# Kernel tuning notes

Hardware: AMD Instinct MI355X
Metric: run time of the kernel (lower is better)

The kernel has to match this reference:

```python
import jax, jax.numpy as jnp
import numpy as np

N = 50000
E = 800000
D_IN = 128
HID = 128
LAT = 64
NEG_SLOPE = 0.2


def setup_inputs() -> dict:
    key = jax.random.key(0)
    ks = jax.random.split(key, 16)
    g = lambda k, shape: jax.random.normal(k, shape, dtype=jnp.float32) * (1.0 / np.sqrt(shape[0]))
    x = jax.random.normal(ks[0], (N, D_IN), dtype=jnp.float32)
    edge_index = jax.random.randint(ks[1], (2, E), 0, N, dtype=jnp.int64)
    return {
        "x": x,
        "edge_index": edge_index,
        # lin1: Linear(D_IN, HID)
        "lin1_w": g(ks[2], (D_IN, HID)),
        "lin1_b": jnp.zeros((HID,), jnp.float32),
        # conv1: GATConv((D_IN, D_IN) -> HID), heads=1
        "w1_src": g(ks[3], (D_IN, HID)),
        "w1_dst": g(ks[4], (D_IN, HID)),
        "a1_src": g(ks[5], (HID,)),
        "a1_dst": g(ks[6], (HID,)),
        "b1": jnp.zeros((HID,), jnp.float32),
        # conv2: GATConv((HID, HID) -> LAT), heads=1
        "w2_src": g(ks[7], (HID, LAT)),
        "w2_dst": g(ks[8], (HID, LAT)),
        "a2_src": g(ks[9], (LAT,)),
        "a2_dst": g(ks[10], (LAT,)),
        "b2": jnp.zeros((LAT,), jnp.float32),
    }


def _gat_conv(x, src, dst, w_src, w_dst, a_src, a_dst, b):
    """PyG GATConv, heads=1, add_self_loops=False. x: [N, Din]."""
    n = x.shape[0]
    hs = x @ w_src                    # [N, C] messages (source transform)
    hd = x @ w_dst                    # [N, C] destination transform
    alpha_s = hs @ a_src              # [N]
    alpha_d = hd @ a_dst              # [N]
    e = jax.nn.leaky_relu(alpha_s[src] + alpha_d[dst], NEG_SLOPE)  # [E]
    # segment softmax over incoming edges per destination node
    m = jax.ops.segment_max(e, dst, num_segments=n)
    ex = jnp.exp(e - m[dst])
    denom = jax.ops.segment_sum(ex, dst, num_segments=n)
    alpha = ex / (denom[dst] + 1e-16)                              # [E]
    msg = hs[src] * alpha[:, None]                                 # [E, C]
    out = jax.ops.segment_sum(msg, dst, num_segments=n)            # [N, C]
    return out + b


def reference(x, edge_index, lin1_w, lin1_b, w1_src, w1_dst, a1_src, a1_dst, b1,
              w2_src, w2_dst, a2_src, a2_dst, b2):
    src, dst = edge_index[0], edge_index[1]
    z = _gat_conv(x, src, dst, w1_src, w1_dst, a1_src, a1_dst, b1)
    z = jax.nn.relu(z + x @ lin1_w + lin1_b)
    z = _gat_conv(z, src, dst, w2_src, w2_dst, a2_src, a2_dst, b2)
    return z
```

## Files before the change

### kernel.cpp

```cpp
#include <hip/hip_runtime.h>

static constexpr int N_NODES = 50000;
static constexpr int N_EDGES = 800000;
static constexpr int NPART = 8;
static constexpr int PART_SZ = N_NODES / NPART;

typedef __attribute__((ext_vector_type(8))) short bf16x8;
typedef __attribute__((ext_vector_type(4))) float f32x4;

__device__ __forceinline__ float bf2f(unsigned short u) {
  union { unsigned int i; float f; } v; v.i = ((unsigned int)u) << 16; return v.f;
}
__device__ __forceinline__ unsigned short f2bf(float f) {
  union { unsigned int i; float f; } v; v.f = f;
  unsigned int r = (v.i + 0x7fffu + ((v.i >> 16) & 1u)) >> 16;
  return (unsigned short)r;
}
__device__ __forceinline__ int clampN(int v) {
  unsigned u = (unsigned)v; return (u < (unsigned)N_NODES) ? (int)u : 0;
}

__global__ void k_detect(const int* __restrict__ ei, int* __restrict__ flag) {
  if (threadIdx.x == 0 && blockIdx.x == 0) {
    int z = ei[1] | ei[3] | ei[5] | ei[7];
    *flag = (z == 0) ? 1 : 0;
  }
}

__global__ void k_zero_out(float* __restrict__ out, int n) {
  int i = blockIdx.x * 256 + threadIdx.x;
  if (i < n) out[i] = 0.f;
}

__global__ void k_prepw(const float* __restrict__ w1_src, const float* __restrict__ wlin,
                        const float* __restrict__ w2_src,
                        const float* __restrict__ w1_dst, const float* __restrict__ a1_dst,
                        const float* __restrict__ w2_dst, const float* __restrict__ a2_dst,
                        unsigned short* __restrict__ w1T, unsigned short* __restrict__ w2T,
                        float* __restrict__ c1dst, float* __restrict__ c2dst) {
  int idx = blockIdx.x * 256 + threadIdx.x;
  if (idx < 256 * 128) {
    int c = idx >> 7, k = idx & 127;
    float v = (c < 128) ? w1_src[k * 128 + c] : wlin[k * 128 + (c - 128)];
    w1T[idx] = f2bf(v);
  } else if (idx < 256 * 128 + 64 * 128) {
    int r = idx - 256 * 128;
    int c = r >> 7, k = r & 127;
    w2T[r] = f2bf(w2_src[k * 64 + c]);
  } else if (blockIdx.x == 160) {
    int k = threadIdx.x;
    if (k < 128) {
      float s1 = 0.f;
      for (int c = 0; c < 128; ++c) s1 += w1_dst[k * 128 + c] * a1_dst[c];
      c1dst[k] = s1;
      float s2 = 0.f;
      for (int c = 0; c < 64; ++c) s2 += w2_dst[k * 64 + c] * a2_dst[c];
      c2dst[k] = s2;
    }
  }
}

__global__ __launch_bounds__(256) void k_gemm1(
    const float* __restrict__ x, const unsigned short* __restrict__ w1T,
    const float* __restrict__ lin_b,
    unsigned short* __restrict__ hs1, unsigned short* __restrict__ linzb) {
  __shared__ unsigned char aLds[16 * 256];
  int nb = blockIdx.x * 16;
  int tid = threadIdx.x;
#pragma unroll
  for (int i = 0; i < 2; ++i) {
    int t = tid + i * 256;
    int row = t >> 5, q = t & 31;
    float4 v = *(const float4*)(x + (size_t)(nb + row) * 128 + q * 4);
    unsigned int lo = (unsigned)f2bf(v.x) | ((unsigned)f2bf(v.y) << 16);
    unsigned int hi = (unsigned)f2bf(v.z) | ((unsigned)f2bf(v.w) << 16);
    int kb = (q * 8) ^ ((row & 7) << 4);
    *(uint2*)(aLds + row * 256 + kb) = make_uint2(lo, hi);
  }
  __syncthreads();
  int wv = tid >> 6, l = tid & 63;
  int lrow = l & 15, lk = l >> 4;
  bf16x8 bfrag[4][4];
#pragma unroll
  for (int ct = 0; ct < 4; ++ct) {
    int col = wv * 64 + ct * 16 + lrow;
#pragma unroll
    for (int ks = 0; ks < 4; ++ks)
      bfrag[ct][ks] = *(const bf16x8*)(w1T + (size_t)col * 128 + ks * 32 + lk * 8);
  }
  f32x4 acc[4] = {{0.f,0.f,0.f,0.f},{0.f,0.f,0.f,0.f},{0.f,0.f,0.f,0.f},{0.f,0.f,0.f,0.f}};
#pragma unroll
  for (int ks = 0; ks < 4; ++ks) {
    int kb = (ks * 64 + lk * 16) ^ ((lrow & 7) << 4);
    bf16x8 afrag = *(const bf16x8*)(aLds + lrow * 256 + kb);
#pragma unroll
    for (int ct = 0; ct < 4; ++ct)
      acc[ct] = __builtin_amdgcn_mfma_f32_16x16x32_bf16(afrag, bfrag[ct][ks], acc[ct], 0, 0, 0);
  }
#pragma unroll
  for (int ct = 0; ct < 4; ++ct) {
    int col = wv * 64 + ct * 16 + lrow;
#pragma unroll
    for (int j = 0; j < 4; ++j) {
      int row = nb + lk * 4 + j;
      float v = acc[ct][j];
      if (col < 128) hs1[(size_t)row * 128 + col] = f2bf(v);
      else linzb[(size_t)row * 128 + (col - 128)] = f2bf(v + lin_b[col - 128]);
    }
  }
}

__global__ __launch_bounds__(256) void k_gemm2(
    const unsigned short* __restrict__ zb, const unsigned short* __restrict__ w2T,
    unsigned short* __restrict__ hs2) {
  __shared__ unsigned char aLds[64 * 256];
  int nb = blockIdx.x * 64;
  int tid = threadIdx.x;
#pragma unroll
  for (int i = 0; i < 4; ++i) {
    int t = tid + i * 256;
    int row = t >> 4, q = t & 15;
    int grow = nb + row; if (grow >= N_NODES) grow = N_NODES - 1;
    uint4 v = *(const uint4*)(zb + (size_t)grow * 128 + q * 8);
    int kb = (q * 16) ^ ((row & 7) << 4);
    *(uint4*)(aLds + row * 256 + kb) = v;
  }
  __syncthreads();
  int wv = tid >> 6, l = tid & 63;
  int lrow = l & 15, lk = l >> 4;
  bf16x8 bfrag[4][4];
#pragma unroll
  for (int ct = 0; ct < 4; ++ct) {
    int col = ct * 16 + lrow;
#pragma unroll
    for (int ks = 0; ks < 4; ++ks)
      bfrag[ct][ks] = *(const bf16x8*)(w2T + (size_t)col * 128 + ks * 32 + lk * 8);
  }
  f32x4 acc[4] = {{0.f,0.f,0.f,0.f},{0.f,0.f,0.f,0.f},{0.f,0.f,0.f,0.f},{0.f,0.f,0.f,0.f}};
  int arow = wv * 16 + lrow;
#pragma unroll
  for (int ks = 0; ks < 4; ++ks) {
    int kb = (ks * 64 + lk * 16) ^ ((arow & 7) << 4);
    bf16x8 afrag = *(const bf16x8*)(aLds + arow * 256 + kb);
#pragma unroll
    for (int ct = 0; ct < 4; ++ct)
      acc[ct] = __builtin_amdgcn_mfma_f32_16x16x32_bf16(afrag, bfrag[ct][ks], acc[ct], 0, 0, 0);
  }
#pragma unroll
  for (int ct = 0; ct < 4; ++ct) {
    int col = ct * 16 + lrow;
#pragma unroll
    for (int j = 0; j < 4; ++j) {
      int row = nb + wv * 16 + lk * 4 + j;
      if (row < N_NODES) hs2[(size_t)row * 64 + col] = f2bf(acc[ct][j]);
    }
  }
}

template <int C, bool XBF>
__global__ __launch_bounds__(256) void k_alpha(
    const unsigned short* __restrict__ hs, const float* __restrict__ asrc,
    const void* __restrict__ xin, const float* __restrict__ cdst,
    float* __restrict__ as_, float* __restrict__ ad_) {
  int node = (int)((blockIdx.x * 256 + threadIdx.x) >> 6);
  if (node >= N_NODES) return;
  int lane = threadIdx.x & 63;
  float sa = 0.f;
#pragma unroll
  for (int k = lane; k < C; k += 64) sa += bf2f(hs[(size_t)node * C + k]) * asrc[k];
  float sd = 0.f;
  if (XBF) {
    const unsigned short* xb = (const unsigned short*)xin;
#pragma unroll
    for (int k = lane; k < 128; k += 64) sd += bf2f(xb[(size_t)node * 128 + k]) * cdst[k];
  } else {
    const float* xf = (const float*)xin;
#pragma unroll
    for (int k = lane; k < 128; k += 64) sd += xf[(size_t)node * 128 + k] * cdst[k];
  }
#pragma unroll
  for (int o = 32; o > 0; o >>= 1) {
    sa += __shfl_xor(sa, o, 64);
    sd += __shfl_xor(sd, o, 64);
  }
  if (lane == 0) { as_[node] = sa; ad_[node] = sd; }
}

__global__ void k_count(const int* __restrict__ ei, const int* __restrict__ flag,
                        int* __restrict__ deg) {
  int part = blockIdx.x & (NPART - 1);
  int e = (blockIdx.x >> 3) * 256 + threadIdx.x;
  if (e < N_EDGES) {
    int f = *flag;
    int d = clampN(ei[(size_t)(N_EDGES + e) << f]);
    int lo = part * PART_SZ;
    if (d >= lo && d < lo + PART_SZ) atomicAdd(&deg[d], 1);
  }
}

__global__ __launch_bounds__(256) void k_scan1(const int* __restrict__ deg,
                                               int* __restrict__ offs,
                                               int* __restrict__ bsums, int n) {
  __shared__ int wsum[4];
  int i = blockIdx.x * 256 + threadIdx.x;
  int lane = threadIdx.x & 63, wid = threadIdx.x >> 6;
  int v = (i < n) ? deg[i] : 0;
  int s = v;
#pragma unroll
  for (int o = 1; o < 64; o <<= 1) { int t = __shfl_up(s, o, 64); if (lane >= o) s += t; }
  if (lane == 63) wsum[wid] = s;
  __syncthreads();
  if (threadIdx.x == 0) {
    int a = 0;
#pragma unroll
    for (int w = 0; w < 4; ++w) { a += wsum[w]; wsum[w] = a; }
  }
  __syncthreads();
  int base = (wid > 0) ? wsum[wid - 1] : 0;
  if (i < n) offs[i] = base + s - v;
  if (threadIdx.x == 0) bsums[blockIdx.x] = wsum[3];
}

__global__ __launch_bounds__(256) void k_scan2(int* __restrict__ bsums, int nb,
                                               int* __restrict__ offs, int n, int etot) {
  __shared__ int wsum[4];
  int tid = threadIdx.x, lane = tid & 63, wid = tid >> 6;
  int v = (tid < nb) ? bsums[tid] : 0;
  int s = v;
#pragma unroll
  for (int o = 1; o < 64; o <<= 1) { int t = __shfl_up(s, o, 64); if (lane >= o) s += t; }
  if (lane == 63) wsum[wid] = s;
  __syncthreads();
  if (tid == 0) {
    int a = 0;
#pragma unroll
    for (int w = 0; w < 4; ++w) { a += wsum[w]; wsum[w] = a; }
  }
  __syncthreads();
  int base = (wid > 0) ? wsum[wid - 1] : 0;
  if (tid < nb) bsums[tid] = base + s - v;
  if (tid == 0) offs[n] = etot;
}

__global__ __launch_bounds__(256) void k_scan3(int* __restrict__ offs, int* __restrict__ cursor,
                                               const int* __restrict__ bsums, int n) {
  int i = blockIdx.x * 256 + threadIdx.x;
  if (i < n) {
    int o = offs[i] + bsums[blockIdx.x];
    offs[i] = o;
    cursor[i] = o;
  }
}

__global__ void k_fill(const int* __restrict__ ei, const int* __restrict__ flag,
                       int* __restrict__ cursor, int* __restrict__ ssrc) {
  int part = blockIdx.x & (NPART - 1);
  int e = (blockIdx.x >> 3) * 256 + threadIdx.x;
  if (e < N_EDGES) {
    int f = *flag;
    int d = clampN(ei[(size_t)(N_EDGES + e) << f]);
    int lo = part * PART_SZ;
    if (d >= lo && d < lo + PART_SZ) {
      int s = clampN(ei[(size_t)e << f]);
      int p = atomicAdd(&cursor[d], 1);
      if ((unsigned)p < (unsigned)N_EDGES) ssrc[p] = s;
    }
  }
}

__global__ __launch_bounds__(256) void k_agg1(
    const int* __restrict__ offs, const int* __restrict__ ssrc,
    const float* __restrict__ as_, const float* __restrict__ ad_,
    const unsigned short* __restrict__ hs1, const float* __restrict__ b1,
    unsigned short* __restrict__ linzb) {
  int node = (int)((blockIdx.x * 256 + threadIdx.x) >> 6);
  if (node >= N_NODES) return;
  int lane = threadIdx.x & 63;
  int g = lane >> 4, cl = lane & 15;
  int o0 = offs[node], o1 = offs[node + 1];
  if (!((unsigned)o0 <= (unsigned)N_EDGES && (unsigned)o1 <= (unsigned)N_EDGES && o0 <= o1))
    { o0 = 0; o1 = 0; }
  int deg = o1 - o0;
  float ad = ad_[node];
  float acc[8];
#pragma unroll
  for (int k = 0; k < 8; ++k) acc[k] = 0.f;
  float ssum = 0.f;
  for (int j = g; j < deg; j += 4) {
    int s = clampN(ssrc[o0 + j]);
    float e = as_[s] + ad;
    e = e > 0.f ? e : 0.2f * e;
    float w = __expf(e);
    uint4 hv = *(const uint4*)(hs1 + (size_t)s * 128 + cl * 8);
    ssum += w;
    acc[0] += w * __uint_as_float(hv.x << 16);
    acc[1] += w * __uint_as_float(hv.x & 0xffff0000u);
    acc[2] += w * __uint_as_float(hv.y << 16);
    acc[3] += w * __uint_as_float(hv.y & 0xffff0000u);
    acc[4] += w * __uint_as_float(hv.z << 16);
    acc[5] += w * __uint_as_float(hv.z & 0xffff0000u);
    acc[6] += w * __uint_as_float(hv.w << 16);
    acc[7] += w * __uint_as_float(hv.w & 0xffff0000u);
  }
  ssum += __shfl_xor(ssum, 16, 64);
  ssum += __shfl_xor(ssum, 32, 64);
#pragma unroll
  for (int k = 0; k < 8; ++k) {
    acc[k] += __shfl_xor(acc[k], 16, 64);
    acc[k] += __shfl_xor(acc[k], 32, 64);
  }
  if (g == 0) {
    float inv = 1.f / (ssum + 1e-16f);
    uint4 lv = *(const uint4*)(linzb + (size_t)node * 128 + cl * 8);
    float4 ba = *(const float4*)(b1 + cl * 8);
    float4 bb = *(const float4*)(b1 + cl * 8 + 4);
    float z[8];
    z[0] = acc[0] * inv + ba.x + __uint_as_float(lv.x << 16);
    z[1] = acc[1] * inv + ba.y + __uint_as_float(lv.x & 0xffff0000u);
    z[2] = acc[2] * inv + ba.z + __uint_as_float(lv.y << 16);
    z[3] = acc[3] * inv + ba.w + __uint_as_float(lv.y & 0xffff0000u);
    z[4] = acc[4] * inv + bb.x + __uint_as_float(lv.z << 16);
    z[5] = acc[5] * inv + bb.y + __uint_as_float(lv.z & 0xffff0000u);
    z[6] = acc[6] * inv + bb.z + __uint_as_float(lv.w << 16);
    z[7] = acc[7] * inv + bb.w + __uint_as_float(lv.w & 0xffff0000u);
#pragma unroll
    for (int k = 0; k < 8; ++k) z[k] = z[k] > 0.f ? z[k] : 0.f;
    uint4 ov;
    ov.x = (unsigned)f2bf(z[0]) | ((unsigned)f2bf(z[1]) << 16);
    ov.y = (unsigned)f2bf(z[2]) | ((unsigned)f2bf(z[3]) << 16);
    ov.z = (unsigned)f2bf(z[4]) | ((unsigned)f2bf(z[5]) << 16);
    ov.w = (unsigned)f2bf(z[6]) | ((unsigned)f2bf(z[7]) << 16);
    *(uint4*)(linzb + (size_t)node * 128 + cl * 8) = ov;
  }
}

__global__ __launch_bounds__(256) void k_agg2(
    const int* __restrict__ offs, const int* __restrict__ ssrc,
    const float* __restrict__ as_, const float* __restrict__ ad_,
    const unsigned short* __restrict__ hs2, const float* __restrict__ b2,
    float* __restrict__ out) {
  int node = (int)((blockIdx.x * 256 + threadIdx.x) >> 6);
  if (node >= N_NODES) return;
  int lane = threadIdx.x & 63;
  int g = lane >> 3, cl = lane & 7;
  int o0 = offs[node], o1 = offs[node + 1];
  if (!((unsigned)o0 <= (unsigned)N_EDGES && (unsigned)o1 <= (unsigned)N_EDGES && o0 <= o1))
    { o0 = 0; o1 = 0; }
  int deg = o1 - o0;
  float ad = ad_[node];
  float acc[8];
#pragma unroll
  for (int k = 0; k < 8; ++k) acc[k] = 0.f;
  float ssum = 0.f;
  for (int j = g; j < deg; j += 8) {
    int s = clampN(ssrc[o0 + j]);
    float e = as_[s] + ad;
    e = e > 0.f ? e : 0.2f * e;
    float w = __expf(e);
    uint4 hv = *(const uint4*)(hs2 + (size_t)s * 64 + cl * 8);
    ssum += w;
    acc[0] += w * __uint_as_float(hv.x << 16);
    acc[1] += w * __uint_as_float(hv.x & 0xffff0000u);
    acc[2] += w * __uint_as_float(hv.y << 16);
    acc[3] += w * __uint_as_float(hv.y & 0xffff0000u);
    acc[4] += w * __uint_as_float(hv.z << 16);
    acc[5] += w * __uint_as_float(hv.z & 0xffff0000u);
    acc[6] += w * __uint_as_float(hv.w << 16);
    acc[7] += w * __uint_as_float(hv.w & 0xffff0000u);
  }
  ssum += __shfl_xor(ssum, 8, 64);
  ssum += __shfl_xor(ssum, 16, 64);
  ssum += __shfl_xor(ssum, 32, 64);
#pragma unroll
  for (int k = 0; k < 8; ++k) {
    acc[k] += __shfl_xor(acc[k], 8, 64);
    acc[k] += __shfl_xor(acc[k], 16, 64);
    acc[k] += __shfl_xor(acc[k], 32, 64);
  }
  if (g == 0) {
    float inv = 1.f / (ssum + 1e-16f);
    float4 ba = *(const float4*)(b2 + cl * 8);
    float4 bb = *(const float4*)(b2 + cl * 8 + 4);
    float4 oa, ob;
    oa.x = acc[0] * inv + ba.x;
    oa.y = acc[1] * inv + ba.y;
    oa.z = acc[2] * inv + ba.z;
    oa.w = acc[3] * inv + ba.w;
    ob.x = acc[4] * inv + bb.x;
    ob.y = acc[5] * inv + bb.y;
    ob.z = acc[6] * inv + bb.z;
    ob.w = acc[7] * inv + bb.w;
    *(float4*)(out + (size_t)node * 64 + cl * 8) = oa;
    *(float4*)(out + (size_t)node * 64 + cl * 8 + 4) = ob;
  }
}

extern "C" void kernel_launch(void* const* d_in, const int* in_sizes, int n_in,
                              void* d_out, int out_size, void* d_ws, size_t ws_size,
                              hipStream_t stream) {
  (void)in_sizes; (void)n_in;
  const float* x      = (const float*)d_in[0];
  const int*   ei     = (const int*)d_in[1];
  const float* lin1_w = (const float*)d_in[2];
  const float* lin1_b = (const float*)d_in[3];
  const float* w1_src = (const float*)d_in[4];
  const float* w1_dst = (const float*)d_in[5];
  const float* a1_src = (const float*)d_in[6];
  const float* a1_dst = (const float*)d_in[7];
  const float* b1     = (const float*)d_in[8];
  const float* w2_src = (const float*)d_in[9];
  const float* w2_dst = (const float*)d_in[10];
  const float* a2_src = (const float*)d_in[11];
  const float* a2_dst = (const float*)d_in[12];
  const float* b2     = (const float*)d_in[13];
  float* out = (float*)d_out;

  char* ws = (char*)d_ws;
  size_t off = 0;
  auto alloc = [&](size_t bytes) -> void* {
    void* p = ws + off;
    off += (bytes + 255) & ~(size_t)255;
    return p;
  };
  int* flag    = (int*)alloc(256);
  float* c1dst = (float*)alloc(128 * 4);
  float* c2dst = (float*)alloc(128 * 4);
  unsigned short* w1T = (unsigned short*)alloc(256 * 128 * 2);
  unsigned short* w2T = (unsigned short*)alloc(64 * 128 * 2);
  int* deg     = (int*)alloc((size_t)N_NODES * 4);
  int* offs    = (int*)alloc((size_t)(N_NODES + 1) * 4);
  int* cursor  = (int*)alloc((size_t)N_NODES * 4);
  int* bsums   = (int*)alloc(1024);
  float* as1   = (float*)alloc((size_t)N_NODES * 4);
  float* ad1   = (float*)alloc((size_t)N_NODES * 4);
  float* as2   = (float*)alloc((size_t)N_NODES * 4);
  float* ad2   = (float*)alloc((size_t)N_NODES * 4);
  int* ssrc    = (int*)alloc((size_t)N_EDGES * 4);
  unsigned short* hs1   = (unsigned short*)alloc((size_t)N_NODES * 128 * 2);
  unsigned short* hs2   = (unsigned short*)alloc((size_t)N_NODES * 64 * 2);
  unsigned short* linzb = (unsigned short*)alloc((size_t)N_NODES * 128 * 2);

  if (off > ws_size) {
    k_zero_out<<<(out_size + 255) / 256, 256, 0, stream>>>(out, out_size);
    return;
  }

  int ebl8 = NPART * ((N_EDGES + 255) / 256);
  int nbl = (N_NODES + 3) / 4;
  hipMemsetAsync(deg, 0, (size_t)N_NODES * 4, stream);
  k_detect<<<1, 64, 0, stream>>>(ei, flag);
  k_prepw<<<161, 256, 0, stream>>>(w1_src, lin1_w, w2_src, w1_dst, a1_dst, w2_dst, a2_dst,
                                   w1T, w2T, c1dst, c2dst);
  k_gemm1<<<N_NODES / 16, 256, 0, stream>>>(x, w1T, lin1_b, hs1, linzb);
  k_alpha<128, false><<<nbl, 256, 0, stream>>>(hs1, a1_src, x, c1dst, as1, ad1);
  k_count<<<ebl8, 256, 0, stream>>>(ei, flag, deg);
  int nb = (N_NODES + 255) / 256;
  k_scan1<<<nb, 256, 0, stream>>>(deg, offs, bsums, N_NODES);
  k_scan2<<<1, 256, 0, stream>>>(bsums, nb, offs, N_NODES, N_EDGES);
  k_scan3<<<nb, 256, 0, stream>>>(offs, cursor, bsums, N_NODES);
  k_fill<<<ebl8, 256, 0, stream>>>(ei, flag, cursor, ssrc);
  k_agg1<<<nbl, 256, 0, stream>>>(offs, ssrc, as1, ad1, hs1, b1, linzb);
  k_gemm2<<<(N_NODES + 63) / 64, 256, 0, stream>>>(linzb, w2T, hs2);
  k_alpha<64, true><<<nbl, 256, 0, stream>>>(hs2, a2_src, linzb, c2dst, as2, ad2);
  k_agg2<<<nbl, 256, 0, stream>>>(offs, ssrc, as2, ad2, hs2, b2, out);
}
```

Before: 223.1 us.

## Fuse attention-score dot products into GEMM epilogues and compact edge indices

Folds the per-node alpha_src and alpha_dst computations into the epilogues of both GEMM kernels, reusing the accumulators and the LDS tile. This removes the two separate k_alpha passes and their re-reads of hs and x. gemm1 is retiled to 64 rows per block, with each wave handling 16 rows across all 256 output columns in four chunks. A k_compact kernel converts the int64-strided edge indices once into int32 src/dst arrays, so k_count and k_fill read contiguous int32 instead of strided 64-bit data. The costs are an extra kernel, 6.4 MB of extra workspace, and higher register pressure in gemm1. ad1 is now computed from bf16-rounded x rather than fp32 x.

```diff
diff --git a/kernel.cpp b/kernel.cpp
--- a/kernel.cpp
+++ b/kernel.cpp
@@ -30,6 +30,16 @@
 __global__ void k_zero_out(float* __restrict__ out, int n) {
   int i = blockIdx.x * 256 + threadIdx.x;
   if (i < n) out[i] = 0.f;
+}
+
+__global__ void k_compact(const int* __restrict__ ei, const int* __restrict__ flag,
+                          int* __restrict__ s32, int* __restrict__ d32) {
+  int e = blockIdx.x * 256 + threadIdx.x;
+  if (e < N_EDGES) {
+    int f = *flag;
+    s32[e] = clampN(ei[(size_t)e << f]);
+    d32[e] = clampN(ei[(size_t)(N_EDGES + e) << f]);
+  }
 }
 
 __global__ void k_prepw(const float* __restrict__ w1_src, const float* __restrict__ wlin,
@@ -62,57 +72,110 @@
 
 __global__ __launch_bounds__(256) void k_gemm1(
     const float* __restrict__ x, const unsigned short* __restrict__ w1T,
-    const float* __restrict__ lin_b,
-    unsigned short* __restrict__ hs1, unsigned short* __restrict__ linzb) {
-  __shared__ unsigned char aLds[16 * 256];
-  int nb = blockIdx.x * 16;
+    const float* __restrict__ lin_b, const float* __restrict__ a1_src,
+    const float* __restrict__ c1dst,
+    unsigned short* __restrict__ hs1, unsigned short* __restrict__ linzb,
+    float* __restrict__ as1, float* __restrict__ ad1) {
+  __shared__ unsigned char aLds[64 * 256];
+  int nb = blockIdx.x * 64;
   int tid = threadIdx.x;
 #pragma unroll
-  for (int i = 0; i < 2; ++i) {
+  for (int i = 0; i < 4; ++i) {
     int t = tid + i * 256;
-    int row = t >> 5, q = t & 31;
-    float4 v = *(const float4*)(x + (size_t)(nb + row) * 128 + q * 4);
-    unsigned int lo = (unsigned)f2bf(v.x) | ((unsigned)f2bf(v.y) << 16);
-    unsigned int hi = (unsigned)f2bf(v.z) | ((unsigned)f2bf(v.w) << 16);
-    int kb = (q * 8) ^ ((row & 7) << 4);
-    *(uint2*)(aLds + row * 256 + kb) = make_uint2(lo, hi);
+    int row = t >> 4, q = t & 15;
+    int grow = nb + row; if (grow >= N_NODES) grow = N_NODES - 1;
+    float4 va = *(const float4*)(x + (size_t)grow * 128 + q * 8);
+    float4 vb = *(const float4*)(x + (size_t)grow * 128 + q * 8 + 4);
+    uint4 o;
+    o.x = (unsigned)f2bf(va.x) | ((unsigned)f2bf(va.y) << 16);
+    o.y = (unsigned)f2bf(va.z) | ((unsigned)f2bf(va.w) << 16);
+    o.z = (unsigned)f2bf(vb.x) | ((unsigned)f2bf(vb.y) << 16);
+    o.w = (unsigned)f2bf(vb.z) | ((unsigned)f2bf(vb.w) << 16);
+    int kb = (q * 16) ^ ((row & 7) << 4);
+    *(uint4*)(aLds + row * 256 + kb) = o;
   }
   __syncthreads();
   int wv = tid >> 6, l = tid & 63;
   int lrow = l & 15, lk = l >> 4;
-  bf16x8 bfrag[4][4];
-#pragma unroll
-  for (int ct = 0; ct < 4; ++ct) {
-    int col = wv * 64 + ct * 16 + lrow;
-#pragma unroll
-    for (int ks = 0; ks < 4; ++ks)
-      bfrag[ct][ks] = *(const bf16x8*)(w1T + (size_t)col * 128 + ks * 32 + lk * 8);
-  }
-  f32x4 acc[4] = {{0.f,0.f,0.f,0.f},{0.f,0.f,0.f,0.f},{0.f,0.f,0.f,0.f},{0.f,0.f,0.f,0.f}};
+  bf16x8 afrag[4];
 #pragma unroll
   for (int ks = 0; ks < 4; ++ks) {
     int kb = (ks * 64 + lk * 16) ^ ((lrow & 7) << 4);
-    bf16x8 afrag = *(const bf16x8*)(aLds + lrow * 256 + kb);
-#pragma unroll
-    for (int ct = 0; ct < 4; ++ct)
-      acc[ct] = __builtin_amdgcn_mfma_f32_16x16x32_bf16(afrag, bfrag[ct][ks], acc[ct], 0, 0, 0);
-  }
-#pragma unroll
-  for (int ct = 0; ct < 4; ++ct) {
-    int col = wv * 64 + ct * 16 + lrow;
+    afrag[ks] = *(const bf16x8*)(aLds + (wv * 16 + lrow) * 256 + kb);
+  }
+  float pa[4] = {0.f, 0.f, 0.f, 0.f};
+#pragma unroll
+  for (int ch = 0; ch < 4; ++ch) {
+    bf16x8 bfrag[4][4];
+#pragma unroll
+    for (int ct = 0; ct < 4; ++ct) {
+      int col = ch * 64 + ct * 16 + lrow;
+#pragma unroll
+      for (int ks = 0; ks < 4; ++ks)
+        bfrag[ct][ks] = *(const bf16x8*)(w1T + (size_t)col * 128 + ks * 32 + lk * 8);
+    }
+    f32x4 acc[4] = {{0.f,0.f,0.f,0.f},{0.f,0.f,0.f,0.f},{0.f,0.f,0.f,0.f},{0.f,0.f,0.f,0.f}};
+#pragma unroll
+    for (int ks = 0; ks < 4; ++ks)
+#pragma unroll
+      for (int ct = 0; ct < 4; ++ct)
+        acc[ct] = __builtin_amdgcn_mfma_f32_16x16x32_bf16(afrag[ks], bfrag[ct][ks], acc[ct], 0, 0, 0);
+#pragma unroll
+    for (int ct = 0; ct < 4; ++ct) {
+      int col = ch * 64 + ct * 16 + lrow;
+      float av = (col < 128) ? a1_src[col] : 0.f;
+#pragma unroll
+      for (int j = 0; j < 4; ++j) {
+        int row = nb + wv * 16 + lk * 4 + j;
+        float v = acc[ct][j];
+        if (row < N_NODES) {
+          if (col < 128) hs1[(size_t)row * 128 + col] = f2bf(v);
+          else linzb[(size_t)row * 128 + (col - 128)] = f2bf(v + lin_b[col - 128]);
+        }
+        if (col < 128) pa[j] += v * av;
+      }
+    }
+  }
+#pragma unroll
+  for (int j = 0; j < 4; ++j) {
+    pa[j] += __shfl_xor(pa[j], 1, 64);
+    pa[j] += __shfl_xor(pa[j], 2, 64);
+    pa[j] += __shfl_xor(pa[j], 4, 64);
+    pa[j] += __shfl_xor(pa[j], 8, 64);
+  }
+  if (lrow == 0) {
 #pragma unroll
     for (int j = 0; j < 4; ++j) {
-      int row = nb + lk * 4 + j;
-      float v = acc[ct][j];
-      if (col < 128) hs1[(size_t)row * 128 + col] = f2bf(v);
-      else linzb[(size_t)row * 128 + (col - 128)] = f2bf(v + lin_b[col - 128]);
-    }
+      int row = nb + wv * 16 + lk * 4 + j;
+      if (row < N_NODES) as1[row] = pa[j];
+    }
+  }
+  {
+    int r = wv * 16 + (l >> 2), kq = l & 3;
+    float sd = 0.f;
+#pragma unroll
+    for (int b = 0; b < 4; ++b) {
+      int kb = (kq * 64 + b * 16) ^ ((r & 7) << 4);
+      bf16x8 v = *(const bf16x8*)(aLds + r * 256 + kb);
+      int k0 = kq * 32 + b * 8;
+      float4 ca = *(const float4*)(c1dst + k0);
+      float4 cb = *(const float4*)(c1dst + k0 + 4);
+      sd += bf2f((unsigned short)v[0]) * ca.x + bf2f((unsigned short)v[1]) * ca.y +
+            bf2f((unsigned short)v[2]) * ca.z + bf2f((unsigned short)v[3]) * ca.w +
+            bf2f((unsigned short)v[4]) * cb.x + bf2f((unsigned short)v[5]) * cb.y +
+            bf2f((unsigned short)v[6]) * cb.z + bf2f((unsigned short)v[7]) * cb.w;
+    }
+    sd += __shfl_xor(sd, 1, 64);
+    sd += __shfl_xor(sd, 2, 64);
+    int row = nb + r;
+    if (kq == 0 && row < N_NODES) ad1[row] = sd;
   }
 }
 
 __global__ __launch_bounds__(256) void k_gemm2(
     const unsigned short* __restrict__ zb, const unsigned short* __restrict__ w2T,
-    unsigned short* __restrict__ hs2) {
+    const float* __restrict__ a2_src, const float* __restrict__ c2dst,
+    unsigned short* __restrict__ hs2, float* __restrict__ as2, float* __restrict__ ad2) {
   __shared__ unsigned char aLds[64 * 256];
   int nb = blockIdx.x * 64;
   int tid = threadIdx.x;
@@ -137,62 +200,67 @@
       bfrag[ct][ks] = *(const bf16x8*)(w2T + (size_t)col * 128 + ks * 32 + lk * 8);
   }
   f32x4 acc[4] = {{0.f,0.f,0.f,0.f},{0.f,0.f,0.f,0.f},{0.f,0.f,0.f,0.f},{0.f,0.f,0.f,0.f}};
-  int arow = wv * 16 + lrow;
 #pragma unroll
   for (int ks = 0; ks < 4; ++ks) {
-    int kb = (ks * 64 + lk * 16) ^ ((arow & 7) << 4);
-    bf16x8 afrag = *(const bf16x8*)(aLds + arow * 256 + kb);
+    int kb = (ks * 64 + lk * 16) ^ ((lrow & 7) << 4);
+    bf16x8 afrag = *(const bf16x8*)(aLds + (wv * 16 + lrow) * 256 + kb);
 #pragma unroll
     for (int ct = 0; ct < 4; ++ct)
       acc[ct] = __builtin_amdgcn_mfma_f32_16x16x32_bf16(afrag, bfrag[ct][ks], acc[ct], 0, 0, 0);
   }
+  float pa[4] = {0.f, 0.f, 0.f, 0.f};
 #pragma unroll
   for (int ct = 0; ct < 4; ++ct) {
     int col = ct * 16 + lrow;
+    float av = a2_src[col];
 #pragma unroll
     for (int j = 0; j < 4; ++j) {
       int row = nb + wv * 16 + lk * 4 + j;
       if (row < N_NODES) hs2[(size_t)row * 64 + col] = f2bf(acc[ct][j]);
-    }
-  }
-}
-
-template <int C, bool XBF>
-__global__ __launch_bounds__(256) void k_alpha(
-    const unsigned short* __restrict__ hs, const float* __restrict__ asrc,
-    const void* __restrict__ xin, const float* __restrict__ cdst,
-    float* __restrict__ as_, float* __restrict__ ad_) {
-  int node = (int)((blockIdx.x * 256 + threadIdx.x) >> 6);
-  if (node >= N_NODES) return;
-  int lane = threadIdx.x & 63;
-  float sa = 0.f;
-#pragma unroll
-  for (int k = lane; k < C; k += 64) sa += bf2f(hs[(size_t)node * C + k]) * asrc[k];
-  float sd = 0.f;
-  if (XBF) {
-    const unsigned short* xb = (const unsigned short*)xin;
-#pragma unroll
-    for (int k = lane; k < 128; k += 64) sd += bf2f(xb[(size_t)node * 128 + k]) * cdst[k];
-  } else {
-    const float* xf = (const float*)xin;
-#pragma unroll
-    for (int k = lane; k < 128; k += 64) sd += xf[(size_t)node * 128 + k] * cdst[k];
-  }
-#pragma unroll
-  for (int o = 32; o > 0; o >>= 1) {
-    sa += __shfl_xor(sa, o, 64);
-    sd += __shfl_xor(sd, o, 64);
-  }
-  if (lane == 0) { as_[node] = sa; ad_[node] = sd; }
-}
-
-__global__ void k_count(const int* __restrict__ ei, const int* __restrict__ flag,
-                        int* __restrict__ deg) {
+      pa[j] += acc[ct][j] * av;
+    }
+  }
+#pragma unroll
+  for (int j = 0; j < 4; ++j) {
+    pa[j] += __shfl_xor(pa[j], 1, 64);
+    pa[j] += __shfl_xor(pa[j], 2, 64);
+    pa[j] += __shfl_xor(pa[j], 4, 64);
+    pa[j] += __shfl_xor(pa[j], 8, 64);
+  }
+  if (lrow == 0) {
+#pragma unroll
+    for (int j = 0; j < 4; ++j) {
+      int row = nb + wv * 16 + lk * 4 + j;
+      if (row < N_NODES) as2[row] = pa[j];
+    }
+  }
+  {
+    int r = wv * 16 + (l >> 2), kq = l & 3;
+    float sd = 0.f;
+#pragma unroll
+    for (int b = 0; b < 4; ++b) {
+      int kb = (kq * 64 + b * 16) ^ ((r & 7) << 4);
+      bf16x8 v = *(const bf16x8*)(aLds + r * 256 + kb);
+      int k0 = kq * 32 + b * 8;
+      float4 ca = *(const float4*)(c2dst + k0);
+      float4 cb = *(const float4*)(c2dst + k0 + 4);
+      sd += bf2f((unsigned short)v[0]) * ca.x + bf2f((unsigned short)v[1]) * ca.y +
+            bf2f((unsigned short)v[2]) * ca.z + bf2f((unsigned short)v[3]) * ca.w +
+            bf2f((unsigned short)v[4]) * cb.x + bf2f((unsigned short)v[5]) * cb.y +
+            bf2f((unsigned short)v[6]) * cb.z + bf2f((unsigned short)v[7]) * cb.w;
+    }
+    sd += __shfl_xor(sd, 1, 64);
+    sd += __shfl_xor(sd, 2, 64);
+    int row = nb + r;
+    if (kq == 0 && row < N_NODES) ad2[row] = sd;
+  }
+}
+
+__global__ void k_count(const int* __restrict__ d32, int* __restrict__ deg) {
   int part = blockIdx.x & (NPART - 1);
   int e = (blockIdx.x >> 3) * 256 + threadIdx.x;
   if (e < N_EDGES) {
-    int f = *flag;
-    int d = clampN(ei[(size_t)(N_EDGES + e) << f]);
+    int d = d32[e];
     int lo = part * PART_SZ;
     if (d >= lo && d < lo + PART_SZ) atomicAdd(&deg[d], 1);
   }
@@ -252,18 +320,16 @@
   }
 }
 
-__global__ void k_fill(const int* __restrict__ ei, const int* __restrict__ flag,
+__global__ void k_fill(const int* __restrict__ s32, const int* __restrict__ d32,
                        int* __restrict__ cursor, int* __restrict__ ssrc) {
   int part = blockIdx.x & (NPART - 1);
   int e = (blockIdx.x >> 3) * 256 + threadIdx.x;
   if (e < N_EDGES) {
-    int f = *flag;
-    int d = clampN(ei[(size_t)(N_EDGES + e) << f]);
+    int d = d32[e];
     int lo = part * PART_SZ;
     if (d >= lo && d < lo + PART_SZ) {
-      int s = clampN(ei[(size_t)e << f]);
       int p = atomicAdd(&cursor[d], 1);
-      if ((unsigned)p < (unsigned)N_EDGES) ssrc[p] = s;
+      if ((unsigned)p < (unsigned)N_EDGES) ssrc[p] = s32[e];
     }
   }
 }
@@ -435,6 +501,8 @@
   float* ad1   = (float*)alloc((size_t)N_NODES * 4);
   float* as2   = (float*)alloc((size_t)N_NODES * 4);
   float* ad2   = (float*)alloc((size_t)N_NODES * 4);
+  int* s32     = (int*)alloc((size_t)N_EDGES * 4);
+  int* d32     = (int*)alloc((size_t)N_EDGES * 4);
   int* ssrc    = (int*)alloc((size_t)N_EDGES * 4);
   unsigned short* hs1   = (unsigned short*)alloc((size_t)N_NODES * 128 * 2);
   unsigned short* hs2   = (unsigned short*)alloc((size_t)N_NODES * 64 * 2);
@@ -445,22 +513,23 @@
     return;
   }
 
-  int ebl8 = NPART * ((N_EDGES + 255) / 256);
-  int nbl = (N_NODES + 3) / 4;
+  int ebl  = (N_EDGES + 255) / 256;
+  int ebl8 = NPART * ebl;
+  int nbl  = (N_NODES + 3) / 4;
+  int gbl  = (N_NODES + 63) / 64;
   hipMemsetAsync(deg, 0, (size_t)N_NODES * 4, stream);
   k_detect<<<1, 64, 0, stream>>>(ei, flag);
   k_prepw<<<161, 256, 0, stream>>>(w1_src, lin1_w, w2_src, w1_dst, a1_dst, w2_dst, a2_dst,
                                    w1T, w2T, c1dst, c2dst);
-  k_gemm1<<<N_NODES / 16, 256, 0, stream>>>(x, w1T, lin1_b, hs1, linzb);
-  k_alpha<128, false><<<nbl, 256, 0, stream>>>(hs1, a1_src, x, c1dst, as1, ad1);
-  k_count<<<ebl8, 256, 0, stream>>>(ei, flag, deg);
+  k_compact<<<ebl, 256, 0, stream>>>(ei, flag, s32, d32);
+  k_gemm1<<<gbl, 256, 0, stream>>>(x, w1T, lin1_b, a1_src, c1dst, hs1, linzb, as1, ad1);
+  k_count<<<ebl8, 256, 0, stream>>>(d32, deg);
   int nb = (N_NODES + 255) / 256;
   k_scan1<<<nb, 256, 0, stream>>>(deg, offs, bsums, N_NODES);
   k_scan2<<<1, 256, 0, stream>>>(bsums, nb, offs, N_NODES, N_EDGES);
   k_scan3<<<nb, 256, 0, stream>>>(offs, cursor, bsums, N_NODES);
-  k_fill<<<ebl8, 256, 0, stream>>>(ei, flag, cursor, ssrc);
+  k_fill<<<ebl8, 256, 0, stream>>>(s32, d32, cursor, ssrc);
   k_agg1<<<nbl, 256, 0, stream>>>(offs, ssrc, as1, ad1, hs1, b1, linzb);
-  k_gemm2<<<(N_NODES + 63) / 64, 256, 0, stream>>>(linzb, w2T, hs2);
-  k_alpha<64, true><<<nbl, 256, 0, stream>>>(hs2, a2_src, linzb, c2dst, as2, ad2);
+  k_gemm2<<<gbl, 256, 0, stream>>>(linzb, w2T, a2_src, c2dst, hs2, as2, ad2);
   k_agg2<<<nbl, 256, 0, stream>>>(offs, ssrc, as2, ad2, hs2, b2, out);
 }
```

Result: no change. 222.7 us (-0.2%).
